# Optimization experiments

Measured on AMD Instinct MI355X. Metric: run time of the kernel, lower is better.

Reference implementation:

```python
import jax, jax.numpy as jnp
import numpy as np

N, DM, F, G, FG = 4096, 512, 128, 8, 16
DH, DE, ES = 128, 256, 4
E = G * ES
GROUP_TOP_K, EXPERT_TOP_K = 2, 2
TEMP = 1.0
LN_EPS = 1e-5


def _ln(x, g, b):
    m = jnp.mean(x, axis=-1, keepdims=True)
    v = jnp.mean((x - m) ** 2, axis=-1, keepdims=True)
    return (x - m) * jax.lax.rsqrt(v + LN_EPS) * g + b


def _topk_softmax(logits, k):
    # faithful to torch _topk_softmax: softmax over top-k values, zeros elsewhere
    vals, idx = jax.lax.top_k(logits, k)
    w = jax.nn.softmax(vals, axis=-1)
    oh = jax.nn.one_hot(idx, logits.shape[-1], dtype=logits.dtype)  # [..., k, E]
    return jnp.einsum('...ke,...k->...e', oh, w)


def setup_inputs() -> dict:
    key = jax.random.key(0)
    ks = iter(jax.random.split(key, 32))
    n = lambda shape, s=0.02: jax.random.normal(next(ks), shape, dtype=jnp.float32) * s
    d = {
        'hidden': jax.random.normal(next(ks), (N, DM), dtype=jnp.float32),
        'feat': jax.random.normal(next(ks), (N, F), dtype=jnp.float32),
        # pre_ln
        'pre_ln_g': jnp.ones((DM,), jnp.float32), 'pre_ln_b': jnp.zeros((DM,), jnp.float32),
        # router_hidden_encoder: LN(DM) -> Lin(DM,DH) -> GELU -> Lin(DH,DH)
        'rh_ln_g': jnp.ones((DM,), jnp.float32), 'rh_ln_b': jnp.zeros((DM,), jnp.float32),
        'rh_w1': n((DM, DH)), 'rh_b1': jnp.zeros((DH,), jnp.float32),
        'rh_w2': n((DH, DH)), 'rh_b2': jnp.zeros((DH,), jnp.float32),
        # stage_feature_encoder: LN(F) -> Lin(F,DH) -> GELU -> Lin(DH,DH)
        'sf_ln_g': jnp.ones((F,), jnp.float32), 'sf_ln_b': jnp.zeros((F,), jnp.float32),
        'sf_w1': n((F, DH)), 'sf_b1': jnp.zeros((DH,), jnp.float32),
        'sf_w2': n((DH, DH)), 'sf_b2': jnp.zeros((DH,), jnp.float32),
        # group_feature_encoders (stacked over G): LN(FG) -> Lin(FG,DH) -> GELU -> Lin(DH,DH)
        'gf_ln_g': jnp.ones((G, FG), jnp.float32), 'gf_ln_b': jnp.zeros((G, FG), jnp.float32),
        'gf_w1': n((G, FG, DH)), 'gf_b1': jnp.zeros((G, DH), jnp.float32),
        'gf_w2': n((G, DH, DH)), 'gf_b2': jnp.zeros((G, DH), jnp.float32),
        # per_group_scorer (ScalarRouter): Lin(4DH,DH) -> GELU -> Lin(DH,1)
        'pgs_w1': n((4 * DH, DH)), 'pgs_b1': jnp.zeros((DH,), jnp.float32),
        'pgs_w2': n((DH,)), 'pgs_b2': jnp.zeros((), jnp.float32),
        # intra_routers (stacked over G): Lin(4DH,DH) -> GELU -> Lin(DH,ES)
        'ir_w1': n((G, 4 * DH, DH)), 'ir_b1': jnp.zeros((G, DH), jnp.float32),
        'ir_w2': n((G, DH, ES)), 'ir_b2': jnp.zeros((G, ES), jnp.float32),
        # experts (stacked over E = G*ES, group-major): Lin(DM,DE) -> GELU -> Lin(DE,DM)
        'ex_w1': n((E, DM, DE)), 'ex_b1': jnp.zeros((E, DE), jnp.float32),
        'ex_w2': n((E, DE, DM)), 'ex_b2': jnp.zeros((E, DM), jnp.float32),
    }
    return d


def reference(hidden, feat, pre_ln_g, pre_ln_b, rh_ln_g, rh_ln_b, rh_w1, rh_b1, rh_w2, rh_b2,
              sf_ln_g, sf_ln_b, sf_w1, sf_b1, sf_w2, sf_b2,
              gf_ln_g, gf_ln_b, gf_w1, gf_b1, gf_w2, gf_b2,
              pgs_w1, pgs_b1, pgs_w2, pgs_b2,
              ir_w1, ir_b1, ir_w2, ir_b2,
              ex_w1, ex_b1, ex_w2, ex_b2):
    # expert input (pre-LN hidden)
    h_norm = _ln(hidden, pre_ln_g, pre_ln_b)                         # [N, DM]

    # factorized router encoders
    h_enc = jax.nn.gelu(_ln(hidden, rh_ln_g, rh_ln_b) @ rh_w1 + rh_b1) @ rh_w2 + rh_b2   # [N, DH]
    s_enc = jax.nn.gelu(_ln(feat, sf_ln_g, sf_ln_b) @ sf_w1 + sf_b1) @ sf_w2 + sf_b2     # [N, DH]
    gfeat = feat.reshape(N, G, FG)                                    # disjoint contiguous group features
    g_h = jax.nn.gelu(jnp.einsum('ngf,gfh->ngh', _ln(gfeat, gf_ln_g, gf_ln_b), gf_w1) + gf_b1)
    g_enc = jnp.einsum('ngh,ghk->ngk', g_h, gf_w2) + gf_b2            # [N, G, DH]

    hB = jnp.broadcast_to(h_enc[:, None, :], (N, G, DH))
    sB = jnp.broadcast_to(s_enc[:, None, :], (N, G, DH))
    router_in = jnp.concatenate([hB, sB, g_enc, hB * g_enc], axis=-1)  # [N, G, 4DH]

    # per-group scalar scores -> group logits -> top-k scatter softmax
    pg_h = jax.nn.gelu(jnp.einsum('ngi,ih->ngh', router_in, pgs_w1) + pgs_b1)
    group_logits = (jnp.einsum('ngh,h->ng', pg_h, pgs_w2) + pgs_b2) / max(TEMP, 1e-6)    # [N, G]
    group_w = _topk_softmax(group_logits, GROUP_TOP_K)                 # [N, G]

    # intra-group expert routers -> top-k scatter softmax over expert_scale
    ir_h = jax.nn.gelu(jnp.einsum('ngi,gih->ngh', router_in, ir_w1) + ir_b1)
    intra_logits = jnp.einsum('ngh,ghe->nge', ir_h, ir_w2) + ir_b2     # [N, G, ES]
    intra_w = _topk_softmax(intra_logits, EXPERT_TOP_K)                # [N, G, ES]

    comb_w = (group_w[:, :, None] * intra_w).reshape(N, E)             # group-major expert order

    # per-expert GELU MLPs on pre-LN hidden (dense compute, sparse weights)
    eh = jax.nn.gelu(jnp.einsum('nd,edh->neh', h_norm, ex_w1) + ex_b1) # [N, E, DE]
    eo = jnp.einsum('neh,ehd->ned', eh, ex_w2) + ex_b2                 # [N, E, DM]
    out = jnp.einsum('ne,ned->nd', comb_w, eo)                         # [N, DM]
    return out
```

## Files before the change

kernel.cpp:

```cpp
#include <hip/hip_runtime.h>
#include <hip/hip_bf16.h>
#include <math.h>

#define N_TOK 4096
#define DM 512
#define FDIM 128
#define G 8
#define FG 16
#define DH 128
#define DE 256
#define ES 4
#define E_EXP 32
#define LN_EPS 1e-5f
#define BT 32

typedef __attribute__((ext_vector_type(8))) short bf16x8;
typedef __attribute__((ext_vector_type(4))) float f32x4;

#define MFMA16(a, b, c) __builtin_amdgcn_mfma_f32_16x16x32_bf16((a), (b), (c), 0, 0, 0)

__device__ __forceinline__ float gelu_t(float x) {
    const float c = 0.7978845608028654f;
    float x3 = x * x * x;
    return 0.5f * x * (1.0f + tanhf(c * (x + 0.044715f * x3)));
}

__device__ __forceinline__ short f2bf(float f) {
    __hip_bfloat16 h = __float2bfloat16(f);
    return *reinterpret_cast<short*>(&h);
}
__device__ __forceinline__ float bf2f(short s) {
    __hip_bfloat16 h = *reinterpret_cast<__hip_bfloat16*>(&s);
    return __bfloat162float(h);
}
__device__ __forceinline__ void split3(float x, short& h, short& m, short& l) {
    h = f2bf(x);
    float r = x - bf2f(h);
    m = f2bf(r);
    float r2 = r - bf2f(m);
    l = f2bf(r2);
}

struct ConvJob { const float* src; short* dh; short* dm; short* dl;
                 int KB, NB, Kreal, plain, blk0; };
struct ConvJobs { ConvJob j[10]; };

__global__ void k_pre(ConvJobs J, int nconv,
                      const float* __restrict__ hidden,
                      const float* __restrict__ pg, const float* __restrict__ pb,
                      const float* __restrict__ rg, const float* __restrict__ rb,
                      __hip_bfloat16* __restrict__ h_normb, float* __restrict__ hL) {
    int b = blockIdx.x;
    if (b >= nconv) {
        int n = b - nconv;
        int j = threadIdx.x;
        const float* x = hidden + (size_t)n * DM;
        float v0 = x[j], v1 = x[j + 256];
        float s = v0 + v1, q = v0 * v0 + v1 * v1;
#pragma unroll
        for (int o = 32; o; o >>= 1) { s += __shfl_down(s, o); q += __shfl_down(q, o); }
        __shared__ float red[8];
        int w = j >> 6;
        if ((j & 63) == 0) { red[w] = s; red[4 + w] = q; }
        __syncthreads();
        float sum = red[0] + red[1] + red[2] + red[3];
        float sq  = red[4] + red[5] + red[6] + red[7];
        float m = sum * (1.0f / DM);
        float var = sq * (1.0f / DM) - m * m;
        float rs = rsqrtf(var + LN_EPS);
        float t0 = (v0 - m) * rs, t1 = (v1 - m) * rs;
        size_t base = (size_t)n * DM;
        h_normb[base + j]       = __float2bfloat16(t0 * pg[j]       + pb[j]);
        h_normb[base + j + 256] = __float2bfloat16(t1 * pg[j + 256] + pb[j + 256]);
        hL[base + j]           = t0 * rg[j]       + rb[j];
        hL[base + j + 256]     = t1 * rg[j + 256] + rb[j + 256];
        return;
    }
    int ji = 0;
#pragma unroll
    for (int i = 1; i < 10; i++) if (b >= J.j[i].blk0) ji = i;
    const ConvJob jb = J.j[ji];
    int rel = b - jb.blk0;
    int mat = rel / jb.KB, kb = rel % jb.KB;
    int ncols = jb.NB * 16;
    const float* s = jb.src + (size_t)mat * jb.Kreal * ncols;
    size_t dbase = ((size_t)mat * jb.KB + kb) * jb.NB * 512;
    for (int p = threadIdx.x; p < jb.NB * 64; p += 256) {
        int nb = p >> 6, lane = p & 63;
        int row0 = kb * 32 + ((lane >> 4) << 3);
        int col = nb * 16 + (lane & 15);
        if (jb.plain) {
            union { short sh[8]; uint4 v; } t;
#pragma unroll
            for (int j = 0; j < 8; j++) {
                float x = (row0 + j < jb.Kreal) ? s[(size_t)(row0 + j) * ncols + col] : 0.f;
                t.sh[j] = f2bf(x);
            }
            *(uint4*)&jb.dh[dbase + (size_t)p * 8] = t.v;
        } else {
            union { short sh[8]; uint4 v; } hi, mi, lo;
#pragma unroll
            for (int j = 0; j < 8; j++) {
                float x = (row0 + j < jb.Kreal) ? s[(size_t)(row0 + j) * ncols + col] : 0.f;
                split3(x, hi.sh[j], mi.sh[j], lo.sh[j]);
            }
            *(uint4*)&jb.dh[dbase + (size_t)p * 8] = hi.v;
            *(uint4*)&jb.dm[dbase + (size_t)p * 8] = mi.v;
            *(uint4*)&jb.dl[dbase + (size_t)p * 8] = lo.v;
        }
    }
}

template <int KB_TOT, bool DO_LN>
__device__ __forceinline__ void enc2_body(
        int bx, char* smem,
        const float* __restrict__ X,
        const float* __restrict__ lng, const float* __restrict__ lnb,
        const short* __restrict__ W1h, const short* __restrict__ W1m, const short* __restrict__ W1l,
        const float* __restrict__ B1,
        const short* __restrict__ W2h, const short* __restrict__ W2m, const short* __restrict__ W2l,
        const float* __restrict__ B2,
        float* __restrict__ Y) {
    constexpr int K = KB_TOT * 32;
    const int n0 = bx * 32;
    const int tid = threadIdx.x;
    const int wave = tid >> 6, lane = tid & 63;
    const int quad = lane >> 4, lm = lane & 15;
    const int mt = wave & 1;
    const int ngb = (wave >> 1) * 4;

    short (*Ah)[132] = (short(*)[132])smem;
    short (*Am)[132] = (short(*)[132])(smem + 32 * 132 * 2);
    short (*Al)[132] = (short(*)[132])(smem + 2 * 32 * 132 * 2);

    f32x4 acc[4];
#pragma unroll
    for (int i = 0; i < 4; i++) acc[i] = (f32x4)(0.f);

    if (DO_LN) {
        for (int idx = tid; idx < 1024; idx += 256) {
            int row = idx >> 5, c4 = (idx & 31) * 4;
            float4 v = *(const float4*)&X[(size_t)(n0 + row) * K + c4];
            float s = v.x + v.y + v.z + v.w;
            float q = v.x * v.x + v.y * v.y + v.z * v.z + v.w * v.w;
#pragma unroll
            for (int o = 16; o; o >>= 1) { s += __shfl_xor(s, o); q += __shfl_xor(q, o); }
            float mean = s * (1.0f / 128.0f);
            float var = q * (1.0f / 128.0f) - mean * mean;
            float rs = rsqrtf(var + LN_EPS);
            float xv[4] = {(v.x - mean) * rs * lng[c4 + 0] + lnb[c4 + 0],
                           (v.y - mean) * rs * lng[c4 + 1] + lnb[c4 + 1],
                           (v.z - mean) * rs * lng[c4 + 2] + lnb[c4 + 2],
                           (v.w - mean) * rs * lng[c4 + 3] + lnb[c4 + 3]};
#pragma unroll
            for (int j = 0; j < 4; j++) {
                short h, m, l; split3(xv[j], h, m, l);
                Ah[row][c4 + j] = h; Am[row][c4 + j] = m; Al[row][c4 + j] = l;
            }
        }
        __syncthreads();
#pragma unroll
        for (int kb = 0; kb < KB_TOT; kb++) {
            bf16x8 ah = *(const bf16x8*)&Ah[mt * 16 + lm][kb * 32 + quad * 8];
            bf16x8 am = *(const bf16x8*)&Am[mt * 16 + lm][kb * 32 + quad * 8];
            bf16x8 al = *(const bf16x8*)&Al[mt * 16 + lm][kb * 32 + quad * 8];
#pragma unroll
            for (int nt = 0; nt < 4; nt++) {
                size_t bi = (((size_t)kb * 8 + ngb + nt) * 64 + lane) * 8;
                bf16x8 bh = *(const bf16x8*)&W1h[bi];
                bf16x8 bm = *(const bf16x8*)&W1m[bi];
                bf16x8 bl = *(const bf16x8*)&W1l[bi];
                acc[nt] = MFMA16(al, bh, acc[nt]);
                acc[nt] = MFMA16(am, bm, acc[nt]);
                acc[nt] = MFMA16(ah, bl, acc[nt]);
                acc[nt] = MFMA16(am, bh, acc[nt]);
                acc[nt] = MFMA16(ah, bm, acc[nt]);
                acc[nt] = MFMA16(ah, bh, acc[nt]);
            }
        }
    } else {
        for (int kb = 0; kb < KB_TOT; kb++) {
            const float* xs = X + (size_t)(n0 + mt * 16 + lm) * K + kb * 32 + quad * 8;
            float4 x0 = *(const float4*)xs, x1 = *(const float4*)(xs + 4);
            float xv[8] = {x0.x, x0.y, x0.z, x0.w, x1.x, x1.y, x1.z, x1.w};
            bf16x8 ah, am, al;
#pragma unroll
            for (int j = 0; j < 8; j++) {
                short h, m, l; split3(xv[j], h, m, l);
                ah[j] = h; am[j] = m; al[j] = l;
            }
#pragma unroll
            for (int nt = 0; nt < 4; nt++) {
                size_t bi = (((size_t)kb * 8 + ngb + nt) * 64 + lane) * 8;
                bf16x8 bh = *(const bf16x8*)&W1h[bi];
                bf16x8 bm = *(const bf16x8*)&W1m[bi];
                bf16x8 bl = *(const bf16x8*)&W1l[bi];
                acc[nt] = MFMA16(al, bh, acc[nt]);
                acc[nt] = MFMA16(am, bm, acc[nt]);
                acc[nt] = MFMA16(ah, bl, acc[nt]);
                acc[nt] = MFMA16(am, bh, acc[nt]);
                acc[nt] = MFMA16(ah, bm, acc[nt]);
                acc[nt] = MFMA16(ah, bh, acc[nt]);
            }
        }
    }
    __syncthreads();
#pragma unroll
    for (int nt = 0; nt < 4; nt++) {
        int col = (ngb + nt) * 16 + lm;
        float b1 = B1[col];
#pragma unroll
        for (int r = 0; r < 4; r++) {
            int row = mt * 16 + quad * 4 + r;
            short h, m, l; split3(gelu_t(acc[nt][r] + b1), h, m, l);
            Ah[row][col] = h; Am[row][col] = m; Al[row][col] = l;
        }
    }
    __syncthreads();
    f32x4 acc2[4];
#pragma unroll
    for (int i = 0; i < 4; i++) acc2[i] = (f32x4)(0.f);
#pragma unroll
    for (int kb = 0; kb < 4; kb++) {
        bf16x8 ah = *(const bf16x8*)&Ah[mt * 16 + lm][kb * 32 + quad * 8];
        bf16x8 am = *(const bf16x8*)&Am[mt * 16 + lm][kb * 32 + quad * 8];
        bf16x8 al = *(const bf16x8*)&Al[mt * 16 + lm][kb * 32 + quad * 8];
#pragma unroll
        for (int nt = 0; nt < 4; nt++) {
            size_t bi = (((size_t)kb * 8 + ngb + nt) * 64 + lane) * 8;
            bf16x8 bh = *(const bf16x8*)&W2h[bi];
            bf16x8 bm = *(const bf16x8*)&W2m[bi];
            bf16x8 bl = *(const bf16x8*)&W2l[bi];
            acc2[nt] = MFMA16(al, bh, acc2[nt]);
            acc2[nt] = MFMA16(am, bm, acc2[nt]);
            acc2[nt] = MFMA16(ah, bl, acc2[nt]);
            acc2[nt] = MFMA16(am, bh, acc2[nt]);
            acc2[nt] = MFMA16(ah, bm, acc2[nt]);
            acc2[nt] = MFMA16(ah, bh, acc2[nt]);
        }
    }
#pragma unroll
    for (int nt = 0; nt < 4; nt++) {
        int col = (ngb + nt) * 16 + lm;
        float b2 = B2[col];
#pragma unroll
        for (int r = 0; r < 4; r++) {
            int row = mt * 16 + quad * 4 + r;
            Y[(size_t)(n0 + row) * DH + col] = acc2[nt][r] + b2;
        }
    }
}

__device__ __forceinline__ void genc_one(
        int bx, int g, char* smem,
        const float* __restrict__ feat,
        const float* __restrict__ gln_g, const float* __restrict__ gln_b,
        const short* __restrict__ W1h, const short* __restrict__ W1m, const short* __restrict__ W1l,
        const float* __restrict__ gb1,
        const short* __restrict__ W2h, const short* __restrict__ W2m, const short* __restrict__ W2l,
        const float* __restrict__ gb2,
        float* __restrict__ g_enc) {
    const int n0 = bx * 32;
    const int tid = threadIdx.x;
    const int wave = tid >> 6, lane = tid & 63;
    const int quad = lane >> 4, lm = lane & 15;
    const int mt = wave & 1;
    const int ngb = (wave >> 1) * 4;

    short (*Ah)[132] = (short(*)[132])smem;
    short (*Am)[132] = (short(*)[132])(smem + 8448);
    short (*Al)[132] = (short(*)[132])(smem + 2 * 8448);

    {
        int t = tid >> 3, sub = tid & 7;
        const float* fr = feat + (size_t)(n0 + t) * FDIM + g * FG;
        float xv[FG];
        float mean = 0.f;
#pragma unroll
        for (int i = 0; i < FG; i++) { xv[i] = fr[i]; mean += xv[i]; }
        mean *= (1.0f / FG);
        float var = 0.f;
#pragma unroll
        for (int i = 0; i < FG; i++) { float d = xv[i] - mean; var += d * d; }
        var *= (1.0f / FG);
        float rs = rsqrtf(var + LN_EPS);
#pragma unroll
        for (int j = 0; j < 2; j++) {
            int i = sub * 2 + j;
            float xn = (xv[i] - mean) * rs * gln_g[g * FG + i] + gln_b[g * FG + i];
            short h, m, l; split3(xn, h, m, l);
            Ah[t][i] = h; Am[t][i] = m; Al[t][i] = l;
            Ah[t][16 + i] = 0; Am[t][16 + i] = 0; Al[t][16 + i] = 0;
        }
    }
    __syncthreads();
    f32x4 acc[4];
#pragma unroll
    for (int i = 0; i < 4; i++) acc[i] = (f32x4)(0.f);
    {
        bf16x8 ah = *(const bf16x8*)&Ah[mt * 16 + lm][quad * 8];
        bf16x8 am = *(const bf16x8*)&Am[mt * 16 + lm][quad * 8];
        bf16x8 al = *(const bf16x8*)&Al[mt * 16 + lm][quad * 8];
#pragma unroll
        for (int nt = 0; nt < 4; nt++) {
            size_t bi = (((size_t)g * 8 + ngb + nt) * 64 + lane) * 8;
            bf16x8 bh = *(const bf16x8*)&W1h[bi];
            bf16x8 bm = *(const bf16x8*)&W1m[bi];
            bf16x8 bl = *(const bf16x8*)&W1l[bi];
            acc[nt] = MFMA16(al, bh, acc[nt]);
            acc[nt] = MFMA16(am, bm, acc[nt]);
            acc[nt] = MFMA16(ah, bl, acc[nt]);
            acc[nt] = MFMA16(am, bh, acc[nt]);
            acc[nt] = MFMA16(ah, bm, acc[nt]);
            acc[nt] = MFMA16(ah, bh, acc[nt]);
        }
    }
    __syncthreads();
#pragma unroll
    for (int nt = 0; nt < 4; nt++) {
        int col = (ngb + nt) * 16 + lm;
        float b1 = gb1[g * DH + col];
#pragma unroll
        for (int r = 0; r < 4; r++) {
            int row = mt * 16 + quad * 4 + r;
            short h, m, l; split3(gelu_t(acc[nt][r] + b1), h, m, l);
            Ah[row][col] = h; Am[row][col] = m; Al[row][col] = l;
        }
    }
    __syncthreads();
    f32x4 acc2[4];
#pragma unroll
    for (int i = 0; i < 4; i++) acc2[i] = (f32x4)(0.f);
#pragma unroll
    for (int kb = 0; kb < 4; kb++) {
        bf16x8 a2h = *(const bf16x8*)&Ah[mt * 16 + lm][kb * 32 + quad * 8];
        bf16x8 a2m = *(const bf16x8*)&Am[mt * 16 + lm][kb * 32 + quad * 8];
        bf16x8 a2l = *(const bf16x8*)&Al[mt * 16 + lm][kb * 32 + quad * 8];
#pragma unroll
        for (int nt = 0; nt < 4; nt++) {
            size_t bi = ((((size_t)g * 4 + kb) * 8 + ngb + nt) * 64 + lane) * 8;
            bf16x8 bh = *(const bf16x8*)&W2h[bi];
            bf16x8 bm = *(const bf16x8*)&W2m[bi];
            bf16x8 bl = *(const bf16x8*)&W2l[bi];
            acc2[nt] = MFMA16(a2l, bh, acc2[nt]);
            acc2[nt] = MFMA16(a2m, bm, acc2[nt]);
            acc2[nt] = MFMA16(a2h, bl, acc2[nt]);
            acc2[nt] = MFMA16(a2m, bh, acc2[nt]);
            acc2[nt] = MFMA16(a2h, bm, acc2[nt]);
            acc2[nt] = MFMA16(a2h, bh, acc2[nt]);
        }
    }
#pragma unroll
    for (int nt = 0; nt < 4; nt++) {
        int col = (ngb + nt) * 16 + lm;
        float b2 = gb2[g * DH + col];
#pragma unroll
        for (int r = 0; r < 4; r++) {
            int row = mt * 16 + quad * 4 + r;
            g_enc[((size_t)(n0 + row) * G + g) * DH + col] = acc2[nt][r] + b2;
        }
    }
}

__global__ __launch_bounds__(256) void k_enc_all(
        const float* __restrict__ hL, const float* __restrict__ feat,
        const float* __restrict__ sf_g, const float* __restrict__ sf_b,
        const float* __restrict__ gln_g, const float* __restrict__ gln_b,
        const short* Brh1H, const short* Brh1M, const short* Brh1L, const float* rh_b1,
        const short* Brh2H, const short* Brh2M, const short* Brh2L, const float* rh_b2,
        const short* Bsf1H, const short* Bsf1M, const short* Bsf1L, const float* sf_b1,
        const short* Bsf2H, const short* Bsf2M, const short* Bsf2L, const float* sf_b2,
        const short* Bgf1H, const short* Bgf1M, const short* Bgf1L, const float* gf_b1,
        const short* Bgf2H, const short* Bgf2M, const short* Bgf2L, const float* gf_b2,
        float* __restrict__ h_enc, float* __restrict__ s_enc, float* __restrict__ g_enc) {
    __shared__ __align__(16) char smem[3 * 8448];
    int bid = blockIdx.x;
    if (bid < 128)
        enc2_body<16, false>(bid, smem, hL, nullptr, nullptr,
                             Brh1H, Brh1M, Brh1L, rh_b1, Brh2H, Brh2M, Brh2L, rh_b2, h_enc);
    else if (bid < 256)
        enc2_body<4, true>(bid - 128, smem, feat, sf_g, sf_b,
                           Bsf1H, Bsf1M, Bsf1L, sf_b1, Bsf2H, Bsf2M, Bsf2L, sf_b2, s_enc);
    else {
        int idx = bid - 256;
        genc_one(idx >> 3, idx & 7, smem, feat, gln_g, gln_b,
                 Bgf1H, Bgf1M, Bgf1L, gf_b1, Bgf2H, Bgf2M, Bgf2L, gf_b2, g_enc);
    }
}

__global__ __launch_bounds__(512) void k_router_mfma(
        const float* __restrict__ h_enc, const float* __restrict__ s_enc,
        const float* __restrict__ g_enc,
        const short* __restrict__ BpgH, const short* __restrict__ BpgM, const short* __restrict__ BpgL,
        const short* __restrict__ BirH, const short* __restrict__ BirM, const short* __restrict__ BirL,
        const float* __restrict__ pb1, const float* __restrict__ pw2, const float* __restrict__ pb2,
        const float* __restrict__ ib1, const float* __restrict__ iw2, const float* __restrict__ ib2,
        float* __restrict__ glog, float* __restrict__ ilog) {
    const int g = blockIdx.x & 7;
    const int bx = blockIdx.x >> 3;
    const int n0 = bx * 64;
    const int tid = threadIdx.x;
    const int wave = tid >> 6, lane = tid & 63;
    const int quad = lane >> 4, lm = lane & 15;
    const bool is_pg = wave < 4;
    const int nbase = (wave & 3) * 2;
    const short* Bh = is_pg ? BpgH : (BirH + (size_t)g * 65536);
    const short* Bm = is_pg ? BpgM : (BirM + (size_t)g * 65536);
    const short* Bl = is_pg ? BpgL : (BirL + (size_t)g * 65536);

    __shared__ __align__(16) char smem[49152];

    f32x4 acc[4][2];
#pragma unroll
    for (int mt = 0; mt < 4; mt++)
#pragma unroll
        for (int nt = 0; nt < 2; nt++) acc[mt][nt] = (f32x4)(0.f);

    for (int ch = 0; ch < 4; ch++) {
        __syncthreads();
        for (int idx = tid; idx < 1024; idx += 512) {
            int kbl = idx >> 8, rem = idx & 255;
            int t16 = rem >> 6, lane2 = rem & 63;
            int gkb = ch * 4 + kbl;
            size_t loff = (size_t)kbl * 4096 + t16 * 1024 + (size_t)lane2 * 16;
            int n = n0 + t16 * 16 + (lane2 & 15);
            int csub = (lane2 >> 4) * 8;
            float xv[8];
            if (gkb < 8) {
                int c0 = gkb * 32 + csub;
                const float* src = (c0 < 128) ? (h_enc + (size_t)n * DH + c0)
                                              : (s_enc + (size_t)n * DH + (c0 - 128));
                float4 x0 = *(const float4*)src, x1 = *(const float4*)(src + 4);
                xv[0]=x0.x; xv[1]=x0.y; xv[2]=x0.z; xv[3]=x0.w;
                xv[4]=x1.x; xv[5]=x1.y; xv[6]=x1.z; xv[7]=x1.w;
            } else {
                int c0 = (gkb - 8) * 32 + csub;
                if (c0 < 128) {
                    const float* gs = g_enc + ((size_t)n * G + g) * DH + c0;
                    float4 x0 = *(const float4*)gs, x1 = *(const float4*)(gs + 4);
                    xv[0]=x0.x; xv[1]=x0.y; xv[2]=x0.z; xv[3]=x0.w;
                    xv[4]=x1.x; xv[5]=x1.y; xv[6]=x1.z; xv[7]=x1.w;
                } else {
                    int c = c0 - 128;
                    const float* gs = g_enc + ((size_t)n * G + g) * DH + c;
                    const float* hsrc = h_enc + (size_t)n * DH + c;
                    float4 g0 = *(const float4*)gs, g1 = *(const float4*)(gs + 4);
                    float4 h0 = *(const float4*)hsrc, h1 = *(const float4*)(hsrc + 4);
                    xv[0]=h0.x*g0.x; xv[1]=h0.y*g0.y; xv[2]=h0.z*g0.z; xv[3]=h0.w*g0.w;
                    xv[4]=h1.x*g1.x; xv[5]=h1.y*g1.y; xv[6]=h1.z*g1.z; xv[7]=h1.w*g1.w;
                }
            }
            union { short sh[8]; uint4 v; } hi, mi, lo;
#pragma unroll
            for (int j = 0; j < 8; j++) split3(xv[j], hi.sh[j], mi.sh[j], lo.sh[j]);
            *(uint4*)(smem + loff)         = hi.v;
            *(uint4*)(smem + 16384 + loff) = mi.v;
            *(uint4*)(smem + 32768 + loff) = lo.v;
        }
        __syncthreads();
#pragma unroll
        for (int kbl = 0; kbl < 4; kbl++) {
            int kb = ch * 4 + kbl;
            bf16x8 Ahf[4], Amf[4], Alf[4];
#pragma unroll
            for (int mt = 0; mt < 4; mt++) {
                size_t loff = (size_t)kbl * 4096 + mt * 1024 + (size_t)lane * 16;
                Ahf[mt] = *(const bf16x8*)(smem + loff);
                Amf[mt] = *(const bf16x8*)(smem + 16384 + loff);
                Alf[mt] = *(const bf16x8*)(smem + 32768 + loff);
            }
#pragma unroll
            for (int nt = 0; nt < 2; nt++) {
                int nb = nbase + nt;
                size_t bi = (((size_t)kb * 8 + nb) * 64 + lane) * 8;
                bf16x8 bh = *(const bf16x8*)&Bh[bi];
                bf16x8 bm = *(const bf16x8*)&Bm[bi];
                bf16x8 bl = *(const bf16x8*)&Bl[bi];
#pragma unroll
                for (int mt = 0; mt < 4; mt++) {
                    acc[mt][nt] = MFMA16(Alf[mt], bh, acc[mt][nt]);
                    acc[mt][nt] = MFMA16(Amf[mt], bm, acc[mt][nt]);
                    acc[mt][nt] = MFMA16(Ahf[mt], bl, acc[mt][nt]);
                    acc[mt][nt] = MFMA16(Amf[mt], bh, acc[mt][nt]);
                    acc[mt][nt] = MFMA16(Ahf[mt], bm, acc[mt][nt]);
                    acc[mt][nt] = MFMA16(Ahf[mt], bh, acc[mt][nt]);
                }
            }
        }
    }

    float (*ph)[129] = (float(*)[129])smem;
    float (*ih)[129] = (float(*)[129])(smem + 32 * 129 * 4);
    for (int h = 0; h < 2; h++) {
        __syncthreads();
#pragma unroll
        for (int mi = 0; mi < 2; mi++) {
            int mt = 2 * h + mi;
#pragma unroll
            for (int nt = 0; nt < 2; nt++) {
                int col = (nbase + nt) * 16 + lm;
                float b1 = is_pg ? pb1[col] : ib1[g * DH + col];
                float* dst = is_pg ? &ph[0][0] : &ih[0][0];
#pragma unroll
                for (int r = 0; r < 4; r++) {
                    int row = mi * 16 + quad * 4 + r;
                    dst[row * 129 + col] = gelu_t(acc[mt][nt][r] + b1);
                }
            }
        }
        __syncthreads();
        if (tid < 32) {
            float s = pb2[0];
            for (int i = 0; i < DH; i++) s += ph[tid][i] * pw2[i];
            glog[(size_t)(n0 + h * 32 + tid) * G + g] = s;
        } else if (tid >= 128 && tid < 256) {
            int t = (tid - 128) >> 2, e = (tid - 128) & 3;
            float s = ib2[g * ES + e];
            const float* w = iw2 + (size_t)g * DH * ES;
            for (int i = 0; i < DH; i++) s += ih[t][i] * w[i * ES + e];
            ilog[((size_t)(n0 + h * 32 + t) * G + g) * ES + e] = s;
        }
    }
}

__global__ void k_topk(const float* __restrict__ glog, const float* __restrict__ ilog,
                       int* __restrict__ cnt, int* __restrict__ toks, float* __restrict__ wgts) {
    int n = blockIdx.x * blockDim.x + threadIdx.x;
    if (n >= N_TOK) return;
    float gl[G];
#pragma unroll
    for (int g = 0; g < G; g++) gl[g] = glog[(size_t)n * G + g];
    int i1 = 0; float v1 = gl[0];
#pragma unroll
    for (int g = 1; g < G; g++) if (gl[g] > v1) { v1 = gl[g]; i1 = g; }
    int i2 = -1; float v2 = -1e30f;
#pragma unroll
    for (int g = 0; g < G; g++) if (g != i1 && gl[g] > v2) { v2 = gl[g]; i2 = g; }
    float eg = expf(v2 - v1);
    float den = 1.0f / (1.0f + eg);
    float gw_sel[2] = { den, eg * den };
    int g_sel[2] = { i1, i2 };
#pragma unroll
    for (int s = 0; s < 2; s++) {
        int g = g_sel[s]; float gw = gw_sel[s];
        float il[ES];
#pragma unroll
        for (int e = 0; e < ES; e++) il[e] = ilog[((size_t)n * G + g) * ES + e];
        int j1 = 0; float u1 = il[0];
#pragma unroll
        for (int e = 1; e < ES; e++) if (il[e] > u1) { u1 = il[e]; j1 = e; }
        int j2 = -1; float u2 = -1e30f;
#pragma unroll
        for (int e = 0; e < ES; e++) if (e != j1 && il[e] > u2) { u2 = il[e]; j2 = e; }
        float ei = expf(u2 - u1);
        float d2 = 1.0f / (1.0f + ei);
        int ex1 = g * ES + j1, ex2 = g * ES + j2;
        int p1 = atomicAdd(&cnt[ex1], 1);
        toks[(size_t)ex1 * N_TOK + p1] = n * 4 + s * 2;     wgts[(size_t)ex1 * N_TOK + p1] = gw * d2;
        int p2 = atomicAdd(&cnt[ex2], 1);
        toks[(size_t)ex2 * N_TOK + p2] = n * 4 + s * 2 + 1; wgts[(size_t)ex2 * N_TOK + p2] = gw * ei * d2;
    }
}

__global__ __launch_bounds__(512) void k_expert_mfma(
        const __hip_bfloat16* __restrict__ h_normb,
        const short* __restrict__ wB1, const float* __restrict__ eb1,
        const short* __restrict__ wB2, const float* __restrict__ eb2,
        const int* __restrict__ cnt, const int* __restrict__ toks,
        const float* __restrict__ wgts, float* __restrict__ part) {
    const int e = blockIdx.x & 31;
    const int slot = blockIdx.x >> 5;
    const int c = cnt[e];
    const int start = slot * BT;
    if (start >= c) return;
    const int m = min(BT, c - start);

    __shared__ short hs[BT][520];
    short (*es)[264] = (short(*)[264])&hs[0][0];
    __shared__ int   tok_s[BT];
    __shared__ float w_s[BT];

    const int tid = threadIdx.x;
    if (tid < BT) {
        bool ok = tid < m;
        tok_s[tid] = ok ? toks[(size_t)e * N_TOK + start + tid] : 0;
        w_s[tid]   = ok ? wgts[(size_t)e * N_TOK + start + tid] : 0.f;
    }
    __syncthreads();
    for (int idx = tid; idx < BT * 64; idx += 512) {
        int t = idx >> 6, ch = idx & 63;
        uint4 v = make_uint4(0, 0, 0, 0);
        if (t < m) v = *((const uint4*)(h_normb + (size_t)(tok_s[t] >> 2) * DM) + ch);
        *(uint4*)&hs[t][ch * 8] = v;
    }
    __syncthreads();

    const int wave = tid >> 6, lane = tid & 63;
    const int quad = lane >> 4, lm = lane & 15;

    const int ng = wave * 2;
    f32x4 acc1[2][2];
#pragma unroll
    for (int a = 0; a < 2; a++)
#pragma unroll
        for (int b = 0; b < 2; b++) acc1[a][b] = (f32x4)(0.f);
    {
        const short* w1e = wB1 + (size_t)e * DM * DE;
        for (int kb = 0; kb < 16; kb++) {
            bf16x8 a0 = *(const bf16x8*)&hs[lm][kb * 32 + quad * 8];
            bf16x8 a1 = *(const bf16x8*)&hs[16 + lm][kb * 32 + quad * 8];
            const short* wp = w1e + ((size_t)kb * 16 + ng) * 512 + lane * 8;
#pragma unroll
            for (int nt = 0; nt < 2; nt++) {
                bf16x8 b = *(const bf16x8*)(wp + nt * 512);
                acc1[0][nt] = MFMA16(a0, b, acc1[0][nt]);
                acc1[1][nt] = MFMA16(a1, b, acc1[1][nt]);
            }
        }
    }
    __syncthreads();
#pragma unroll
    for (int nt = 0; nt < 2; nt++) {
        int col = (ng + nt) * 16 + lm;
        float b1 = eb1[e * DE + col];
#pragma unroll
        for (int mt = 0; mt < 2; mt++)
#pragma unroll
        for (int r = 0; r < 4; r++) {
            int row = mt * 16 + quad * 4 + r;
            es[row][col] = f2bf(gelu_t(acc1[mt][nt][r] + b1));
        }
    }
    __syncthreads();

    {
        const int ng2 = wave * 4;
        f32x4 acc[2][4];
#pragma unroll
        for (int a = 0; a < 2; a++)
#pragma unroll
            for (int b = 0; b < 4; b++) acc[a][b] = (f32x4)(0.f);
        const short* w2e = wB2 + (size_t)e * DE * DM;
        for (int kb = 0; kb < 8; kb++) {
            bf16x8 a0 = *(const bf16x8*)&es[lm][kb * 32 + quad * 8];
            bf16x8 a1 = *(const bf16x8*)&es[16 + lm][kb * 32 + quad * 8];
            const short* wp = w2e + ((size_t)kb * 32 + ng2) * 512 + lane * 8;
#pragma unroll
            for (int nt = 0; nt < 4; nt++) {
                bf16x8 b = *(const bf16x8*)(wp + nt * 512);
                acc[0][nt] = MFMA16(a0, b, acc[0][nt]);
                acc[1][nt] = MFMA16(a1, b, acc[1][nt]);
            }
        }
        const float* b2 = eb2 + (size_t)e * DM;
#pragma unroll
        for (int mt = 0; mt < 2; mt++)
#pragma unroll
        for (int r = 0; r < 4; r++) {
            int row = mt * 16 + quad * 4 + r;
            if (row < m) {
                float w = w_s[row];
                float* prow = part + (size_t)tok_s[row] * DM;
#pragma unroll
                for (int nt = 0; nt < 4; nt++) {
                    int col = (ng2 + nt) * 16 + lm;
                    prow[col] = w * (acc[mt][nt][r] + b2[col]);
                }
            }
        }
    }
}

__global__ void k_reduce(const float* __restrict__ part, float* __restrict__ out) {
    int n = blockIdx.x;
    int j = threadIdx.x;
    const float4* p = (const float4*)(part + (size_t)n * 4 * DM);
    float4 a = p[j], b = p[128 + j], c = p[256 + j], d = p[384 + j];
    float4 r = make_float4(a.x + b.x + c.x + d.x, a.y + b.y + c.y + d.y,
                           a.z + b.z + c.z + d.z, a.w + b.w + c.w + d.w);
    ((float4*)(out + (size_t)n * DM))[j] = r;
}

extern "C" void kernel_launch(void* const* d_in, const int* in_sizes, int n_in,
                              void* d_out, int out_size, void* d_ws, size_t ws_size,
                              hipStream_t stream) {
    const float* hidden  = (const float*)d_in[0];
    const float* feat    = (const float*)d_in[1];
    const float* pre_g   = (const float*)d_in[2];
    const float* pre_b   = (const float*)d_in[3];
    const float* rh_g    = (const float*)d_in[4];
    const float* rh_b    = (const float*)d_in[5];
    const float* rh_w1   = (const float*)d_in[6];
    const float* rh_b1   = (const float*)d_in[7];
    const float* rh_w2   = (const float*)d_in[8];
    const float* rh_b2   = (const float*)d_in[9];
    const float* sf_g    = (const float*)d_in[10];
    const float* sf_b    = (const float*)d_in[11];
    const float* sf_w1   = (const float*)d_in[12];
    const float* sf_b1   = (const float*)d_in[13];
    const float* sf_w2   = (const float*)d_in[14];
    const float* sf_b2   = (const float*)d_in[15];
    const float* gln_g   = (const float*)d_in[16];
    const float* gln_b   = (const float*)d_in[17];
    const float* gf_w1   = (const float*)d_in[18];
    const float* gf_b1   = (const float*)d_in[19];
    const float* gf_w2   = (const float*)d_in[20];
    const float* gf_b2   = (const float*)d_in[21];
    const float* pgs_w1  = (const float*)d_in[22];
    const float* pgs_b1  = (const float*)d_in[23];
    const float* pgs_w2  = (const float*)d_in[24];
    const float* pgs_b2  = (const float*)d_in[25];
    const float* ir_w1   = (const float*)d_in[26];
    const float* ir_b1   = (const float*)d_in[27];
    const float* ir_w2   = (const float*)d_in[28];
    const float* ir_b2   = (const float*)d_in[29];
    const float* ex_w1   = (const float*)d_in[30];
    const float* ex_b1   = (const float*)d_in[31];
    const float* ex_w2   = (const float*)d_in[32];
    const float* ex_b2   = (const float*)d_in[33];
    float* out = (float*)d_out;

    char* w = (char*)d_ws;
    auto alloc = [&](size_t bytes) { void* r = (void*)w; w += (bytes + 255) & ~(size_t)255; return r; };
    __hip_bfloat16* h_normb = (__hip_bfloat16*)alloc((size_t)N_TOK * DM * 2);
    float* h_enc = (float*)alloc((size_t)N_TOK * DH * 4);
    float* s_enc = (float*)alloc((size_t)N_TOK * DH * 4);
    float* g_enc = (float*)alloc((size_t)N_TOK * G * DH * 4);
    float* glog  = (float*)alloc((size_t)N_TOK * G * 4);
    float* ilog  = (float*)alloc((size_t)N_TOK * G * ES * 4);
    float* wgts  = (float*)alloc((size_t)E_EXP * N_TOK * 4);
    short* wB1   = (short*)alloc((size_t)E_EXP * DM * DE * 2);
    short* wB2   = (short*)alloc((size_t)E_EXP * DE * DM * 2);
    short* BpgH  = (short*)alloc((size_t)16 * 8 * 512 * 2);
    short* BpgM  = (short*)alloc((size_t)16 * 8 * 512 * 2);
    short* BpgL  = (short*)alloc((size_t)16 * 8 * 512 * 2);
    short* BirH  = (short*)alloc((size_t)G * 16 * 8 * 512 * 2);
    short* BirM  = (short*)alloc((size_t)G * 16 * 8 * 512 * 2);
    short* BirL  = (short*)alloc((size_t)G * 16 * 8 * 512 * 2);
    short* Brh1H = (short*)alloc((size_t)16 * 8 * 512 * 2);
    short* Brh1M = (short*)alloc((size_t)16 * 8 * 512 * 2);
    short* Brh1L = (short*)alloc((size_t)16 * 8 * 512 * 2);
    short* Brh2H = (short*)alloc((size_t)4 * 8 * 512 * 2);
    short* Brh2M = (short*)alloc((size_t)4 * 8 * 512 * 2);
    short* Brh2L = (short*)alloc((size_t)4 * 8 * 512 * 2);
    short* Bsf1H = (short*)alloc((size_t)4 * 8 * 512 * 2);
    short* Bsf1M = (short*)alloc((size_t)4 * 8 * 512 * 2);
    short* Bsf1L = (short*)alloc((size_t)4 * 8 * 512 * 2);
    short* Bsf2H = (short*)alloc((size_t)4 * 8 * 512 * 2);
    short* Bsf2M = (short*)alloc((size_t)4 * 8 * 512 * 2);
    short* Bsf2L = (short*)alloc((size_t)4 * 8 * 512 * 2);
    short* Bgf1H = (short*)alloc((size_t)G * 1 * 8 * 512 * 2);
    short* Bgf1M = (short*)alloc((size_t)G * 1 * 8 * 512 * 2);
    short* Bgf1L = (short*)alloc((size_t)G * 1 * 8 * 512 * 2);
    short* Bgf2H = (short*)alloc((size_t)G * 4 * 8 * 512 * 2);
    short* Bgf2M = (short*)alloc((size_t)G * 4 * 8 * 512 * 2);
    short* Bgf2L = (short*)alloc((size_t)G * 4 * 8 * 512 * 2);
    int* cnt     = (int*)alloc(E_EXP * 4);
    int* toks    = (int*)alloc((size_t)E_EXP * N_TOK * 4);
    char* uni   = (char*)alloc((size_t)N_TOK * 4 * DM * 4);
    float* hL   = (float*)uni;
    float* part = (float*)uni;

    hipMemsetAsync(cnt, 0, E_EXP * sizeof(int), stream);

    ConvJobs J;
    int b0 = 0;
    auto mkjob = [&](int i, const float* s, short* dh, short* dm, short* dl,
                     int KB, int NB, int Kreal, int plain, int nmat) {
        J.j[i] = ConvJob{s, dh, dm, dl, KB, NB, Kreal, plain, b0};
        b0 += KB * nmat;
    };
    mkjob(0, ex_w1, wB1, nullptr, nullptr, 16, 16, 512, 1, E_EXP);
    mkjob(1, ex_w2, wB2, nullptr, nullptr, 8, 32, 256, 1, E_EXP);
    mkjob(2, pgs_w1, BpgH, BpgM, BpgL, 16, 8, 512, 0, 1);
    mkjob(3, ir_w1, BirH, BirM, BirL, 16, 8, 512, 0, G);
    mkjob(4, rh_w1, Brh1H, Brh1M, Brh1L, 16, 8, 512, 0, 1);
    mkjob(5, rh_w2, Brh2H, Brh2M, Brh2L, 4, 8, 128, 0, 1);
    mkjob(6, sf_w1, Bsf1H, Bsf1M, Bsf1L, 4, 8, 128, 0, 1);
    mkjob(7, sf_w2, Bsf2H, Bsf2M, Bsf2L, 4, 8, 128, 0, 1);
    mkjob(8, gf_w1, Bgf1H, Bgf1M, Bgf1L, 1, 8, 16, 0, G);
    mkjob(9, gf_w2, Bgf2H, Bgf2M, Bgf2L, 4, 8, 128, 0, G);
    k_pre<<<b0 + N_TOK, 256, 0, stream>>>(J, b0, hidden, pre_g, pre_b, rh_g, rh_b, h_normb, hL);

    k_enc_all<<<256 + (N_TOK / 32) * G, 256, 0, stream>>>(
        hL, feat, sf_g, sf_b, gln_g, gln_b,
        Brh1H, Brh1M, Brh1L, rh_b1, Brh2H, Brh2M, Brh2L, rh_b2,
        Bsf1H, Bsf1M, Bsf1L, sf_b1, Bsf2H, Bsf2M, Bsf2L, sf_b2,
        Bgf1H, Bgf1M, Bgf1L, gf_b1, Bgf2H, Bgf2M, Bgf2L, gf_b2,
        h_enc, s_enc, g_enc);

    k_router_mfma<<<(N_TOK / 64) * G, 512, 0, stream>>>(h_enc, s_enc, g_enc,
                                             BpgH, BpgM, BpgL, BirH, BirM, BirL,
                                             pgs_b1, pgs_w2, pgs_b2, ir_b1, ir_w2, ir_b2,
                                             glog, ilog);

    k_topk<<<N_TOK / 256, 256, 0, stream>>>(glog, ilog, cnt, toks, wgts);
    k_expert_mfma<<<(N_TOK / BT) * E_EXP, 512, 0, stream>>>(h_normb, wB1, ex_b1, wB2, ex_b2,
                                                            cnt, toks, wgts, part);
    k_reduce<<<N_TOK, 128, 0, stream>>>(part, out);
}
```

Measured before the change: 325.0 us.

## Emit encoder outputs as pre-split bf16 MFMA tiles and stream them via LDS

The encoder kernels now split their fp32 outputs into hi/mid/lo bf16 parts and write them in the MFMA fragment tile layout the router consumes, instead of writing plain fp32 rows. The router loads three of its four K-chunks straight into LDS with global_load_lds, which removes the per-element split3 work and the strided fp32 gathers. The h*g chunk is rebuilt from the split parts. The router's final dot products are also spread across more threads with shuffle reductions. The cost is extra LDS staging and barriers in the encoders, more bytes written for the three-way split, and reuse of the hL scratch region for Gs.

```diff
diff --git a/kernel.cpp b/kernel.cpp
--- a/kernel.cpp
+++ b/kernel.cpp
@@ -19,6 +19,8 @@
 
 #define MFMA16(a, b, c) __builtin_amdgcn_mfma_f32_16x16x32_bf16((a), (b), (c), 0, 0, 0)
 
+#define PSTRIDE 6144
+
 __device__ __forceinline__ float gelu_t(float x) {
     const float c = 0.7978845608028654f;
     float x3 = x * x * x;
@@ -39,6 +41,12 @@
     m = f2bf(r);
     float r2 = r - bf2f(m);
     l = f2bf(r2);
+}
+
+__device__ __forceinline__ void gload_lds16(const void* g, void* l) {
+    __builtin_amdgcn_global_load_lds(
+        (const __attribute__((address_space(1))) unsigned int*)g,
+        (__attribute__((address_space(3))) unsigned int*)l, 16, 0, 0);
 }
 
 struct ConvJob { const float* src; short* dh; short* dm; short* dl;
@@ -111,6 +119,21 @@
     }
 }
 
+__device__ __forceinline__ void emit_split_tiles(
+        int tid, short (*Ah)[136], short (*Am)[136], short (*Al)[136],
+        short* __restrict__ Yt, size_t panel0 ) {
+    int lane_ = tid & 63, w = tid >> 6;
+#pragma unroll
+    for (int j = 0; j < 6; j++) {
+        int combo = w * 6 + j;
+        int split = combo >> 3;
+        int rem = combo & 7; int t16 = rem >> 2, kb = rem & 3;
+        const short* sp = (split == 0) ? &Ah[0][0] : (split == 1) ? &Am[0][0] : &Al[0][0];
+        uint4 v = *(const uint4*)&sp[(t16 * 16 + (lane_ & 15)) * 136 + kb * 32 + (lane_ >> 4) * 8];
+        *(uint4*)&Yt[((panel0 + t16) * 4 + kb) * 1536 + split * 512 + lane_ * 8] = v;
+    }
+}
+
 template <int KB_TOT, bool DO_LN>
 __device__ __forceinline__ void enc2_body(
         int bx, char* smem,
@@ -120,7 +143,7 @@
         const float* __restrict__ B1,
         const short* __restrict__ W2h, const short* __restrict__ W2m, const short* __restrict__ W2l,
         const float* __restrict__ B2,
-        float* __restrict__ Y) {
+        short* __restrict__ Yt) {
     constexpr int K = KB_TOT * 32;
     const int n0 = bx * 32;
     const int tid = threadIdx.x;
@@ -129,9 +152,9 @@
     const int mt = wave & 1;
     const int ngb = (wave >> 1) * 4;
 
-    short (*Ah)[132] = (short(*)[132])smem;
-    short (*Am)[132] = (short(*)[132])(smem + 32 * 132 * 2);
-    short (*Al)[132] = (short(*)[132])(smem + 2 * 32 * 132 * 2);
+    short (*Ah)[136] = (short(*)[136])smem;
+    short (*Am)[136] = (short(*)[136])(smem + 8704);
+    short (*Al)[136] = (short(*)[136])(smem + 2 * 8704);
 
     f32x4 acc[4];
 #pragma unroll
@@ -239,6 +262,7 @@
             acc2[nt] = MFMA16(ah, bh, acc2[nt]);
         }
     }
+    __syncthreads();
 #pragma unroll
     for (int nt = 0; nt < 4; nt++) {
         int col = (ngb + nt) * 16 + lm;
@@ -246,9 +270,12 @@
 #pragma unroll
         for (int r = 0; r < 4; r++) {
             int row = mt * 16 + quad * 4 + r;
-            Y[(size_t)(n0 + row) * DH + col] = acc2[nt][r] + b2;
-        }
-    }
+            short h, m, l; split3(acc2[nt][r] + b2, h, m, l);
+            Ah[row][col] = h; Am[row][col] = m; Al[row][col] = l;
+        }
+    }
+    __syncthreads();
+    emit_split_tiles(tid, Ah, Am, Al, Yt, (size_t)bx * 2);
 }
 
 __device__ __forceinline__ void genc_one(
@@ -259,17 +286,17 @@
         const float* __restrict__ gb1,
         const short* __restrict__ W2h, const short* __restrict__ W2m, const short* __restrict__ W2l,
         const float* __restrict__ gb2,
-        float* __restrict__ g_enc) {
-    const int n0 = bx * 32;
+        short* __restrict__ Gs) {
     const int tid = threadIdx.x;
     const int wave = tid >> 6, lane = tid & 63;
     const int quad = lane >> 4, lm = lane & 15;
     const int mt = wave & 1;
     const int ngb = (wave >> 1) * 4;
-
-    short (*Ah)[132] = (short(*)[132])smem;
-    short (*Am)[132] = (short(*)[132])(smem + 8448);
-    short (*Al)[132] = (short(*)[132])(smem + 2 * 8448);
+    const int n0 = bx * 32;
+
+    short (*Ah)[136] = (short(*)[136])smem;
+    short (*Am)[136] = (short(*)[136])(smem + 8704);
+    short (*Al)[136] = (short(*)[136])(smem + 2 * 8704);
 
     {
         int t = tid >> 3, sub = tid & 7;
@@ -350,6 +377,7 @@
             acc2[nt] = MFMA16(a2h, bh, acc2[nt]);
         }
     }
+    __syncthreads();
 #pragma unroll
     for (int nt = 0; nt < 4; nt++) {
         int col = (ngb + nt) * 16 + lm;
@@ -357,9 +385,12 @@
 #pragma unroll
         for (int r = 0; r < 4; r++) {
             int row = mt * 16 + quad * 4 + r;
-            g_enc[((size_t)(n0 + row) * G + g) * DH + col] = acc2[nt][r] + b2;
-        }
-    }
+            short h, m, l; split3(acc2[nt][r] + b2, h, m, l);
+            Ah[row][col] = h; Am[row][col] = m; Al[row][col] = l;
+        }
+    }
+    __syncthreads();
+    emit_split_tiles(tid, Ah, Am, Al, Gs, (size_t)g * 256 + bx * 2);
 }
 
 __global__ __launch_bounds__(256) void k_enc_all(
@@ -372,25 +403,24 @@
         const short* Bsf2H, const short* Bsf2M, const short* Bsf2L, const float* sf_b2,
         const short* Bgf1H, const short* Bgf1M, const short* Bgf1L, const float* gf_b1,
         const short* Bgf2H, const short* Bgf2M, const short* Bgf2L, const float* gf_b2,
-        float* __restrict__ h_enc, float* __restrict__ s_enc, float* __restrict__ g_enc) {
-    __shared__ __align__(16) char smem[3 * 8448];
+        short* __restrict__ Hs, short* __restrict__ Ss, short* __restrict__ Gs) {
+    __shared__ __align__(16) char smem[3 * 8704];
     int bid = blockIdx.x;
     if (bid < 128)
         enc2_body<16, false>(bid, smem, hL, nullptr, nullptr,
-                             Brh1H, Brh1M, Brh1L, rh_b1, Brh2H, Brh2M, Brh2L, rh_b2, h_enc);
+                             Brh1H, Brh1M, Brh1L, rh_b1, Brh2H, Brh2M, Brh2L, rh_b2, Hs);
     else if (bid < 256)
         enc2_body<4, true>(bid - 128, smem, feat, sf_g, sf_b,
-                           Bsf1H, Bsf1M, Bsf1L, sf_b1, Bsf2H, Bsf2M, Bsf2L, sf_b2, s_enc);
+                           Bsf1H, Bsf1M, Bsf1L, sf_b1, Bsf2H, Bsf2M, Bsf2L, sf_b2, Ss);
     else {
         int idx = bid - 256;
         genc_one(idx >> 3, idx & 7, smem, feat, gln_g, gln_b,
-                 Bgf1H, Bgf1M, Bgf1L, gf_b1, Bgf2H, Bgf2M, Bgf2L, gf_b2, g_enc);
+                 Bgf1H, Bgf1M, Bgf1L, gf_b1, Bgf2H, Bgf2M, Bgf2L, gf_b2, Gs);
     }
 }
 
 __global__ __launch_bounds__(512) void k_router_mfma(
-        const float* __restrict__ h_enc, const float* __restrict__ s_enc,
-        const float* __restrict__ g_enc,
+        const short* __restrict__ Hs, const short* __restrict__ Ss, const short* __restrict__ Gs,
         const short* __restrict__ BpgH, const short* __restrict__ BpgM, const short* __restrict__ BpgL,
         const short* __restrict__ BirH, const short* __restrict__ BirM, const short* __restrict__ BirL,
         const float* __restrict__ pb1, const float* __restrict__ pw2, const float* __restrict__ pb2,
@@ -408,6 +438,10 @@
     const short* Bm = is_pg ? BpgM : (BirM + (size_t)g * 65536);
     const short* Bl = is_pg ? BpgL : (BirL + (size_t)g * 65536);
 
+    const short* HsB = Hs + (size_t)bx * 4 * PSTRIDE;
+    const short* SsB = Ss + (size_t)bx * 4 * PSTRIDE;
+    const short* GsB = Gs + ((size_t)g * 256 + bx * 4) * PSTRIDE;
+
     __shared__ __align__(16) char smem[49152];
 
     f32x4 acc[4][2];
@@ -418,44 +452,41 @@
 
     for (int ch = 0; ch < 4; ch++) {
         __syncthreads();
-        for (int idx = tid; idx < 1024; idx += 512) {
-            int kbl = idx >> 8, rem = idx & 255;
-            int t16 = rem >> 6, lane2 = rem & 63;
-            int gkb = ch * 4 + kbl;
-            size_t loff = (size_t)kbl * 4096 + t16 * 1024 + (size_t)lane2 * 16;
-            int n = n0 + t16 * 16 + (lane2 & 15);
-            int csub = (lane2 >> 4) * 8;
-            float xv[8];
-            if (gkb < 8) {
-                int c0 = gkb * 32 + csub;
-                const float* src = (c0 < 128) ? (h_enc + (size_t)n * DH + c0)
-                                              : (s_enc + (size_t)n * DH + (c0 - 128));
-                float4 x0 = *(const float4*)src, x1 = *(const float4*)(src + 4);
-                xv[0]=x0.x; xv[1]=x0.y; xv[2]=x0.z; xv[3]=x0.w;
-                xv[4]=x1.x; xv[5]=x1.y; xv[6]=x1.z; xv[7]=x1.w;
-            } else {
-                int c0 = (gkb - 8) * 32 + csub;
-                if (c0 < 128) {
-                    const float* gs = g_enc + ((size_t)n * G + g) * DH + c0;
-                    float4 x0 = *(const float4*)gs, x1 = *(const float4*)(gs + 4);
-                    xv[0]=x0.x; xv[1]=x0.y; xv[2]=x0.z; xv[3]=x0.w;
-                    xv[4]=x1.x; xv[5]=x1.y; xv[6]=x1.z; xv[7]=x1.w;
-                } else {
-                    int c = c0 - 128;
-                    const float* gs = g_enc + ((size_t)n * G + g) * DH + c;
-                    const float* hsrc = h_enc + (size_t)n * DH + c;
-                    float4 g0 = *(const float4*)gs, g1 = *(const float4*)(gs + 4);
-                    float4 h0 = *(const float4*)hsrc, h1 = *(const float4*)(hsrc + 4);
-                    xv[0]=h0.x*g0.x; xv[1]=h0.y*g0.y; xv[2]=h0.z*g0.z; xv[3]=h0.w*g0.w;
-                    xv[4]=h1.x*g1.x; xv[5]=h1.y*g1.y; xv[6]=h1.z*g1.z; xv[7]=h1.w*g1.w;
+        if (ch < 3) {
+            const short* base = (ch == 0) ? HsB : (ch == 1) ? SsB : GsB;
+#pragma unroll
+            for (int it = 0; it < 6; it++) {
+                int combo = wave * 6 + it;
+                int split = combo >> 4;
+                int rem = combo & 15; int kbl = rem >> 2, t16 = rem & 3;
+                const short* gp = base + (size_t)t16 * PSTRIDE + kbl * 1536 + split * 512 + lane * 8;
+                char* lp = smem + split * 16384 + kbl * 4096 + t16 * 1024;
+                gload_lds16(gp, lp);
+            }
+        } else {
+            for (int idx = tid; idx < 1024; idx += 512) {
+                int kbl = idx >> 8, rem = idx & 255;
+                int t16 = rem >> 6, lane2 = rem & 63;
+                size_t loff = (size_t)kbl * 4096 + t16 * 1024 + (size_t)lane2 * 16;
+                bf16x8 gh = *(const bf16x8*)(smem + loff);
+                bf16x8 gm = *(const bf16x8*)(smem + 16384 + loff);
+                bf16x8 gl = *(const bf16x8*)(smem + 32768 + loff);
+                const short* hp = HsB + (size_t)t16 * PSTRIDE + kbl * 1536 + lane2 * 8;
+                bf16x8 hh8 = *(const bf16x8*)hp;
+                bf16x8 hm8 = *(const bf16x8*)(hp + 512);
+                bf16x8 hl8 = *(const bf16x8*)(hp + 1024);
+                union { short sh[8]; uint4 v; } oh, om, ol;
+#pragma unroll
+                for (int j = 0; j < 8; j++) {
+                    float gv = bf2f(gh[j]) + bf2f(gm[j]) + bf2f(gl[j]);
+                    float hv = bf2f(hh8[j]) + bf2f(hm8[j]) + bf2f(hl8[j]);
+                    short a_, b_, c_; split3(hv * gv, a_, b_, c_);
+                    oh.sh[j] = a_; om.sh[j] = b_; ol.sh[j] = c_;
                 }
-            }
-            union { short sh[8]; uint4 v; } hi, mi, lo;
-#pragma unroll
-            for (int j = 0; j < 8; j++) split3(xv[j], hi.sh[j], mi.sh[j], lo.sh[j]);
-            *(uint4*)(smem + loff)         = hi.v;
-            *(uint4*)(smem + 16384 + loff) = mi.v;
-            *(uint4*)(smem + 32768 + loff) = lo.v;
+                *(uint4*)(smem + loff) = oh.v;
+                *(uint4*)(smem + 16384 + loff) = om.v;
+                *(uint4*)(smem + 32768 + loff) = ol.v;
+            }
         }
         __syncthreads();
 #pragma unroll
@@ -509,16 +540,21 @@
             }
         }
         __syncthreads();
-        if (tid < 32) {
-            float s = pb2[0];
-            for (int i = 0; i < DH; i++) s += ph[tid][i] * pw2[i];
-            glog[(size_t)(n0 + h * 32 + tid) * G + g] = s;
-        } else if (tid >= 128 && tid < 256) {
-            int t = (tid - 128) >> 2, e = (tid - 128) & 3;
-            float s = ib2[g * ES + e];
-            const float* w = iw2 + (size_t)g * DH * ES;
-            for (int i = 0; i < DH; i++) s += ih[t][i] * w[i * ES + e];
-            ilog[((size_t)(n0 + h * 32 + t) * G + g) * ES + e] = s;
+        if (tid < 128) {
+            int t = tid >> 2, q = tid & 3;
+            float s = 0.f;
+            for (int i = q * 32; i < q * 32 + 32; i++) s += ph[t][i] * pw2[i];
+            s += __shfl_xor(s, 1);
+            s += __shfl_xor(s, 2);
+            if (q == 0) glog[(size_t)(n0 + h * 32 + t) * G + g] = s + pb2[0];
+        } else if (tid < 384) {
+            int t2 = tid - 128;
+            int t = t2 >> 3, e = (t2 >> 1) & 3, half = t2 & 1;
+            const float* wv = iw2 + (size_t)g * DH * ES;
+            float s = 0.f;
+            for (int i = half * 64; i < half * 64 + 64; i++) s += ih[t][i] * wv[i * ES + e];
+            s += __shfl_xor(s, 1);
+            if (half == 0) ilog[((size_t)(n0 + h * 32 + t) * G + g) * ES + e] = s + ib2[g * ES + e];
         }
     }
 }
@@ -723,9 +759,8 @@
     char* w = (char*)d_ws;
     auto alloc = [&](size_t bytes) { void* r = (void*)w; w += (bytes + 255) & ~(size_t)255; return r; };
     __hip_bfloat16* h_normb = (__hip_bfloat16*)alloc((size_t)N_TOK * DM * 2);
-    float* h_enc = (float*)alloc((size_t)N_TOK * DH * 4);
-    float* s_enc = (float*)alloc((size_t)N_TOK * DH * 4);
-    float* g_enc = (float*)alloc((size_t)N_TOK * G * DH * 4);
+    short* Hs    = (short*)alloc((size_t)256 * PSTRIDE * 2);
+    short* Ss    = (short*)alloc((size_t)256 * PSTRIDE * 2);
     float* glog  = (float*)alloc((size_t)N_TOK * G * 4);
     float* ilog  = (float*)alloc((size_t)N_TOK * G * ES * 4);
     float* wgts  = (float*)alloc((size_t)E_EXP * N_TOK * 4);
@@ -759,6 +794,7 @@
     int* toks    = (int*)alloc((size_t)E_EXP * N_TOK * 4);
     char* uni   = (char*)alloc((size_t)N_TOK * 4 * DM * 4);
     float* hL   = (float*)uni;
+    short* Gs   = (short*)(uni + (size_t)N_TOK * DM * 4);
     float* part = (float*)uni;
 
     hipMemsetAsync(cnt, 0, E_EXP * sizeof(int), stream);
@@ -787,9 +823,9 @@
         Brh1H, Brh1M, Brh1L, rh_b1, Brh2H, Brh2M, Brh2L, rh_b2,
         Bsf1H, Bsf1M, Bsf1L, sf_b1, Bsf2H, Bsf2M, Bsf2L, sf_b2,
         Bgf1H, Bgf1M, Bgf1L, gf_b1, Bgf2H, Bgf2M, Bgf2L, gf_b2,
-        h_enc, s_enc, g_enc);
-
-    k_router_mfma<<<(N_TOK / 64) * G, 512, 0, stream>>>(h_enc, s_enc, g_enc,
+        Hs, Ss, Gs);
+
+    k_router_mfma<<<(N_TOK / 64) * G, 512, 0, stream>>>(Hs, Ss, Gs,
                                              BpgH, BpgM, BpgL, BirH, BirM, BirL,
                                              pgs_b1, pgs_w2, pgs_b2, ir_b1, ir_w2, ir_b2,
                                              glog, ilog);
```

New measurement: 339.0 us. +4.3%, slower.

## Fuse expert combine via atomicAdd into output and parallelize router logit dots

Applied to the files above, without the earlier changes.

Each expert block now atomically accumulates its weighted output straight into the zeroed output buffer. This removes the per-token partial buffer and the separate k_reduce pass. Separately, the final router scalar and intra-logit dot products are split across more threads and combined with wave shuffles, which shortens a serial 128-length loop. The cost is float atomics on the output (roughly four per element), a memset of the output, and a summation order that is no longer deterministic.

```diff
diff --git a/kernel.cpp b/kernel.cpp
--- a/kernel.cpp
+++ b/kernel.cpp
@@ -260,12 +260,12 @@
         const short* __restrict__ W2h, const short* __restrict__ W2m, const short* __restrict__ W2l,
         const float* __restrict__ gb2,
         float* __restrict__ g_enc) {
-    const int n0 = bx * 32;
     const int tid = threadIdx.x;
     const int wave = tid >> 6, lane = tid & 63;
     const int quad = lane >> 4, lm = lane & 15;
     const int mt = wave & 1;
     const int ngb = (wave >> 1) * 4;
+    const int n0 = bx * 32;
 
     short (*Ah)[132] = (short(*)[132])smem;
     short (*Am)[132] = (short(*)[132])(smem + 8448);
@@ -509,16 +509,21 @@
             }
         }
         __syncthreads();
-        if (tid < 32) {
-            float s = pb2[0];
-            for (int i = 0; i < DH; i++) s += ph[tid][i] * pw2[i];
-            glog[(size_t)(n0 + h * 32 + tid) * G + g] = s;
-        } else if (tid >= 128 && tid < 256) {
-            int t = (tid - 128) >> 2, e = (tid - 128) & 3;
-            float s = ib2[g * ES + e];
-            const float* w = iw2 + (size_t)g * DH * ES;
-            for (int i = 0; i < DH; i++) s += ih[t][i] * w[i * ES + e];
-            ilog[((size_t)(n0 + h * 32 + t) * G + g) * ES + e] = s;
+        if (tid < 128) {
+            int t = tid >> 2, q = tid & 3;
+            float s = 0.f;
+            for (int i = q * 32; i < q * 32 + 32; i++) s += ph[t][i] * pw2[i];
+            s += __shfl_xor(s, 1);
+            s += __shfl_xor(s, 2);
+            if (q == 0) glog[(size_t)(n0 + h * 32 + t) * G + g] = s + pb2[0];
+        } else if (tid < 384) {
+            int t2 = tid - 128;
+            int t = t2 >> 3, e = (t2 >> 1) & 3, half = t2 & 1;
+            const float* wv = iw2 + (size_t)g * DH * ES;
+            float s = 0.f;
+            for (int i = half * 64; i < half * 64 + 64; i++) s += ih[t][i] * wv[i * ES + e];
+            s += __shfl_xor(s, 1);
+            if (half == 0) ilog[((size_t)(n0 + h * 32 + t) * G + g) * ES + e] = s + ib2[g * ES + e];
         }
     }
 }
@@ -556,9 +561,9 @@
         float d2 = 1.0f / (1.0f + ei);
         int ex1 = g * ES + j1, ex2 = g * ES + j2;
         int p1 = atomicAdd(&cnt[ex1], 1);
-        toks[(size_t)ex1 * N_TOK + p1] = n * 4 + s * 2;     wgts[(size_t)ex1 * N_TOK + p1] = gw * d2;
+        toks[(size_t)ex1 * N_TOK + p1] = n;     wgts[(size_t)ex1 * N_TOK + p1] = gw * d2;
         int p2 = atomicAdd(&cnt[ex2], 1);
-        toks[(size_t)ex2 * N_TOK + p2] = n * 4 + s * 2 + 1; wgts[(size_t)ex2 * N_TOK + p2] = gw * ei * d2;
+        toks[(size_t)ex2 * N_TOK + p2] = n;     wgts[(size_t)ex2 * N_TOK + p2] = gw * ei * d2;
     }
 }
 
@@ -567,7 +572,7 @@
         const short* __restrict__ wB1, const float* __restrict__ eb1,
         const short* __restrict__ wB2, const float* __restrict__ eb2,
         const int* __restrict__ cnt, const int* __restrict__ toks,
-        const float* __restrict__ wgts, float* __restrict__ part) {
+        const float* __restrict__ wgts, float* __restrict__ out) {
     const int e = blockIdx.x & 31;
     const int slot = blockIdx.x >> 5;
     const int c = cnt[e];
@@ -590,7 +595,7 @@
     for (int idx = tid; idx < BT * 64; idx += 512) {
         int t = idx >> 6, ch = idx & 63;
         uint4 v = make_uint4(0, 0, 0, 0);
-        if (t < m) v = *((const uint4*)(h_normb + (size_t)(tok_s[t] >> 2) * DM) + ch);
+        if (t < m) v = *((const uint4*)(h_normb + (size_t)tok_s[t] * DM) + ch);
         *(uint4*)&hs[t][ch * 8] = v;
     }
     __syncthreads();
@@ -660,25 +665,15 @@
             int row = mt * 16 + quad * 4 + r;
             if (row < m) {
                 float w = w_s[row];
-                float* prow = part + (size_t)tok_s[row] * DM;
+                float* orow = out + (size_t)tok_s[row] * DM;
 #pragma unroll
                 for (int nt = 0; nt < 4; nt++) {
                     int col = (ng2 + nt) * 16 + lm;
-                    prow[col] = w * (acc[mt][nt][r] + b2[col]);
+                    atomicAdd(&orow[col], w * (acc[mt][nt][r] + b2[col]));
                 }
             }
         }
     }
-}
-
-__global__ void k_reduce(const float* __restrict__ part, float* __restrict__ out) {
-    int n = blockIdx.x;
-    int j = threadIdx.x;
-    const float4* p = (const float4*)(part + (size_t)n * 4 * DM);
-    float4 a = p[j], b = p[128 + j], c = p[256 + j], d = p[384 + j];
-    float4 r = make_float4(a.x + b.x + c.x + d.x, a.y + b.y + c.y + d.y,
-                           a.z + b.z + c.z + d.z, a.w + b.w + c.w + d.w);
-    ((float4*)(out + (size_t)n * DM))[j] = r;
 }
 
 extern "C" void kernel_launch(void* const* d_in, const int* in_sizes, int n_in,
@@ -757,11 +752,10 @@
     short* Bgf2L = (short*)alloc((size_t)G * 4 * 8 * 512 * 2);
     int* cnt     = (int*)alloc(E_EXP * 4);
     int* toks    = (int*)alloc((size_t)E_EXP * N_TOK * 4);
-    char* uni   = (char*)alloc((size_t)N_TOK * 4 * DM * 4);
-    float* hL   = (float*)uni;
-    float* part = (float*)uni;
+    float* hL    = (float*)alloc((size_t)N_TOK * DM * 4);
 
     hipMemsetAsync(cnt, 0, E_EXP * sizeof(int), stream);
+    hipMemsetAsync(out, 0, (size_t)N_TOK * DM * sizeof(float), stream);
 
     ConvJobs J;
     int b0 = 0;
@@ -796,6 +790,5 @@
 
     k_topk<<<N_TOK / 256, 256, 0, stream>>>(glog, ilog, cnt, toks, wgts);
     k_expert_mfma<<<(N_TOK / BT) * E_EXP, 512, 0, stream>>>(h_normb, wB1, ex_b1, wB2, ex_b2,
-                                                            cnt, toks, wgts, part);
-    k_reduce<<<N_TOK, 128, 0, stream>>>(part, out);
-}
+                                                            cnt, toks, wgts, out);
+}
```

Result: slower. 358.3 us (+10.2%).
